# Kernel tuning notes

Hardware: AMD Instinct MI355X
Metric: run time of the kernel (lower is better)

The kernel has to match this reference:

```python
import jax, jax.numpy as jnp
import numpy as np

NUM_EXPERTS = 64
TOP_K = 2
AUX_LOSS_COEF = 0.01
Z_LOSS_COEF = 0.001


def setup_inputs() -> dict:
    key = jax.random.key(0)
    k1, k2 = jax.random.split(key)
    hidden_states = jax.random.normal(k1, (4, 4096, 4096), dtype=jnp.float32)
    # nn.Linear(hidden_size, num_experts, bias=False) -> weight [E, H]
    gate_w = jax.random.normal(k2, (NUM_EXPERTS, 4096), dtype=jnp.float32) * 0.02
    return {"hidden_states": hidden_states, "gate_w": gate_w}


def reference(hidden_states, gate_w):
    b, s, h = hidden_states.shape
    # gate projection: [b, s, E]
    router_logits = jnp.einsum("bsh,eh->bse", hidden_states, gate_w)
    # softmax in fp32 as in the torch module
    probs = jax.nn.softmax(router_logits.astype(jnp.float32), axis=-1)
    routing_weights, selected_experts = jax.lax.top_k(probs, TOP_K)
    routing_weights = routing_weights / jnp.sum(routing_weights, axis=-1, keepdims=True)
    routing_weights = routing_weights.astype(hidden_states.dtype)

    # auxiliary load-balancing loss
    num_tokens = b * s
    # scatter_(-1, selected, 1): top-k indices are distinct, so one_hot-sum == set-to-1
    expert_mask = jax.nn.one_hot(selected_experts, NUM_EXPERTS, dtype=router_logits.dtype).sum(axis=-2)  # [b,s,E]
    tokens_per_expert = expert_mask.sum(axis=(0, 1)) / num_tokens          # [E]
    router_prob_per_expert = probs.sum(axis=(0, 1)) / num_tokens           # [E]
    aux_loss = NUM_EXPERTS * jnp.sum(tokens_per_expert * router_prob_per_expert)

    # z-loss: mean of squared logsumexp over experts
    z_loss = jnp.mean(jax.scipy.special.logsumexp(router_logits, axis=-1) ** 2)

    router_loss = AUX_LOSS_COEF * aux_loss + Z_LOSS_COEF * z_loss
    return routing_weights, selected_experts, router_loss
```

## Files before the change

### kernel.cpp

```cpp
#include <hip/hip_runtime.h>
#include <math.h>

#define HDIM 4096
#define NEXP 64
#define NTOK 16384
#define MBLK 32
#define NCHUNK 64
#define CSTRIDE 68
#define GS_FLOATS 262144

typedef float v4f __attribute__((ext_vector_type(4)));
typedef short bh4 __attribute__((ext_vector_type(4)));
typedef float f32x16 __attribute__((ext_vector_type(16)));

#if defined(__has_builtin)
#if __has_builtin(__builtin_amdgcn_mfma_f32_32x32x8bf16_1k)
#define HAVE_MFMA_BUILTIN 1
#endif
#endif

__device__ __forceinline__ f32x16 mfma_bf16(bh4 a, bh4 b, f32x16 c) {
#ifdef HAVE_MFMA_BUILTIN
    return __builtin_amdgcn_mfma_f32_32x32x8bf16_1k(a, b, c, 0, 0, 0);
#else
    asm("v_mfma_f32_32x32x8_bf16 %0, %1, %2, %0" : "+v"(c) : "v"(a), "v"(b));
    return c;
#endif
}

__device__ __forceinline__ void barrier_lgkm_only() {
    asm volatile("s_waitcnt lgkmcnt(0)\n\ts_barrier" ::: "memory");
}

__device__ __forceinline__ void split2(float v, unsigned short& h0,
                                       unsigned short& h1) {
    unsigned b0 = __builtin_bit_cast(unsigned, v);
    unsigned r0 = (b0 + 0x7FFFu + ((b0 >> 16) & 1u)) & 0xFFFF0000u;
    h0 = (unsigned short)(r0 >> 16);
    float v1 = v - __builtin_bit_cast(float, r0);
    unsigned b1 = __builtin_bit_cast(unsigned, v1);
    h1 = (unsigned short)((b1 + 0x7FFFu + ((b1 >> 16) & 1u)) >> 16);
}

__device__ __forceinline__ uint2 pack4(const unsigned short* h) {
    return make_uint2((unsigned)h[0] | ((unsigned)h[1] << 16),
                      (unsigned)h[2] | ((unsigned)h[3] << 16));
}

__global__ __launch_bounds__(256) void gate_presplit(
    const float* __restrict__ gate, uint2* __restrict__ gs)
{
    const int f = blockIdx.x * 256 + threadIdx.x;
    const int l = f & 63;
    const int ntp = (f >> 6) & 1;
    const int k8g = f >> 7;
    const int e = ntp * 32 + (l & 31);
    const int k = k8g * 8 + (l >> 5) * 4;
    v4f x = *(const v4f*)&gate[(size_t)e * HDIM + k];
    float xv[4] = {x.x, x.y, x.z, x.w};
    unsigned short lo[4], hi[4];
#pragma unroll
    for (int j = 0; j < 4; ++j) split2(xv[j], lo[j], hi[j]);
    gs[((size_t)(k8g * 2 + 0) * 2 + ntp) * 64 + l] = pack4(lo);
    gs[((size_t)(k8g * 2 + 1) * 2 + ntp) * 64 + l] = pack4(hi);
}

__global__ __launch_bounds__(256, 4) void router_main(
    const float* __restrict__ hidden,
    const uint2* __restrict__ gs,
    float* __restrict__ out_rw,
    float* __restrict__ out_sel,
    float* __restrict__ psum_g,
    float* __restrict__ cnt_g,
    float* __restrict__ zsum_g)
{
    __shared__ uint2 Af[2][8][2][64];
    __shared__ float Pacc[2][16][64];
    __shared__ float C_lds[MBLK * CSTRIDE];
    __shared__ float rden[MBLK];
    __shared__ unsigned hist[NEXP];

    const int t = threadIdx.x;
    const int lane = t & 63;
    const int wave = __builtin_amdgcn_readfirstlane(t >> 6);
    const int ntp = wave & 1, h = wave >> 1;
    const int m0 = blockIdx.x * MBLK;

    const v4f* __restrict__ A4 = (const v4f*)hidden;

    const int row = t >> 3;
    const int k8s = t & 7;
    const size_t abase = (size_t)(m0 + row) * (HDIM / 4) + k8s * 2;
    const int sw_w = (k8s & 1) << 3;

    auto stageA = [&](int buf, v4f x0, v4f x1) {
        float av[8] = {x0.x, x0.y, x0.z, x0.w, x1.x, x1.y, x1.z, x1.w};
        unsigned short lo[8], hi[8];
#pragma unroll
        for (int u = 0; u < 8; ++u) split2(av[u], lo[u], hi[u]);
        const int s0 = row ^ sw_w;
        Af[buf][k8s][0][s0]      = pack4(lo);
        Af[buf][k8s][0][s0 + 32] = pack4(lo + 4);
        Af[buf][k8s][1][s0]      = pack4(hi);
        Af[buf][k8s][1][s0 + 32] = pack4(hi + 4);
    };

    f32x16 acc{};

    v4f ap0 = __builtin_nontemporal_load(&A4[abase]);
    v4f ap1 = __builtin_nontemporal_load(&A4[abase + 1]);
    stageA(0, ap0, ap1);
    ap0 = __builtin_nontemporal_load(&A4[abase + 16]);
    ap1 = __builtin_nontemporal_load(&A4[abase + 17]);

    uint2 bA[8], bB[8];
#pragma unroll
    for (int s = 0; s < 4; ++s) {
        const int k8g = h * 4 + s;
        bA[2 * s + 0] = gs[((size_t)(k8g * 2 + 0) * 2 + ntp) * 64 + lane];
        bA[2 * s + 1] = gs[((size_t)(k8g * 2 + 1) * 2 + ntp) * 64 + lane];
    }
    __syncthreads();

    auto step = [&](int it, uint2 (&bc)[8], uint2 (&bn)[8]) {
        const int cur = it & 1;
        const int cn = (it + 1 < NCHUNK) ? it + 1 : NCHUNK - 1;
#pragma unroll
        for (int s = 0; s < 4; ++s) {
            const int k8g = cn * 8 + h * 4 + s;
            bn[2 * s + 0] = gs[((size_t)(k8g * 2 + 0) * 2 + ntp) * 64 + lane];
            bn[2 * s + 1] = gs[((size_t)(k8g * 2 + 1) * 2 + ntp) * 64 + lane];
        }
        if (it + 1 < NCHUNK) stageA(cur ^ 1, ap0, ap1);
        const int ca = (it + 2 < NCHUNK) ? it + 2 : NCHUNK - 1;
        ap0 = __builtin_nontemporal_load(&A4[abase + (size_t)ca * 16]);
        ap1 = __builtin_nontemporal_load(&A4[abase + (size_t)ca * 16 + 1]);
#pragma unroll
        for (int s = 0; s < 4; ++s) {
            const int k8 = h * 4 + s;
            const int slot = lane ^ ((k8 & 1) << 3);
            bh4 a0 = __builtin_bit_cast(bh4, Af[cur][k8][0][slot]);
            bh4 a1 = __builtin_bit_cast(bh4, Af[cur][k8][1][slot]);
            bh4 b0 = __builtin_bit_cast(bh4, bc[2 * s + 0]);
            bh4 b1 = __builtin_bit_cast(bh4, bc[2 * s + 1]);
            acc = mfma_bf16(a0, b0, acc);
            acc = mfma_bf16(a1, b0, acc);
            acc = mfma_bf16(a0, b1, acc);
            acc = mfma_bf16(a1, b1, acc);
        }
        barrier_lgkm_only();
    };

    for (int it = 0; it < NCHUNK; it += 2) {
        step(it, bA, bB);
        step(it + 1, bB, bA);
    }

    asm volatile("s_nop 7\n\ts_nop 7" :::);

    if (h == 1) {
#pragma unroll
        for (int r = 0; r < 16; ++r) Pacc[ntp][r][lane] = acc[r];
    }
    if (t < NEXP) hist[t] = 0u;
    __syncthreads();
    if (h == 0) {
#pragma unroll
        for (int r = 0; r < 16; ++r) {
            float x = acc[r] + Pacc[ntp][r][lane];
            const int tok = (r & 3) + 8 * (r >> 2) + 4 * (lane >> 5);
            const int e = ntp * 32 + (lane & 31);
            C_lds[tok * CSTRIDE + e] = x;
        }
    }
    __syncthreads();

    if (wave != 0) return;

    float z = 0.f;
    if (lane < MBLK) {
        float v1 = -INFINITY, v2 = -INFINITY;
        int i1 = 0, i2 = 0;
        for (int e = 0; e < NEXP; ++e) {
            float v = C_lds[lane * CSTRIDE + e];
            if (v > v1)      { v2 = v1; i2 = i1; v1 = v; i1 = e; }
            else if (v > v2) { v2 = v;  i2 = e; }
        }
        atomicAdd(&hist[i1], 1u);
        atomicAdd(&hist[i2], 1u);

        float d = 0.f;
        for (int e = 0; e < NEXP; ++e) {
            float ev = expf(C_lds[lane * CSTRIDE + e] - v1);
            C_lds[lane * CSTRIDE + e] = ev;
            d += ev;
        }
        rden[lane] = 1.0f / d;
        float lse = v1 + logf(d);
        z = lse * lse;

        float e2 = expf(v2 - v1);
        float w2 = e2 / (1.f + e2);
        float w1 = 1.f - w2;
        int tok = m0 + lane;
        out_rw[2 * tok + 0] = w1;
        out_rw[2 * tok + 1] = w2;
        out_sel[2 * tok + 0] = (float)i1;
        out_sel[2 * tok + 1] = (float)i2;
    }

#pragma unroll
    for (int off = 32; off > 0; off >>= 1) z += __shfl_down(z, off);
    if (lane == 0) atomicAdd(zsum_g, z);

    float ps = 0.f;
    for (int m = 0; m < MBLK; ++m)
        ps += C_lds[m * CSTRIDE + lane] * rden[m];
    atomicAdd(&psum_g[lane], ps);
    atomicAdd(&cnt_g[lane], (float)hist[lane]);
}

__global__ void router_final(const float* __restrict__ ws, float* __restrict__ out_loss)
{
    int e = threadIdx.x;
    const float inv = 1.0f / (float)NTOK;
    float p = (ws[64 + e] * inv) * (ws[e] * inv);
#pragma unroll
    for (int off = 32; off > 0; off >>= 1) p += __shfl_down(p, off);
    if (e == 0)
        out_loss[0] = 0.01f * (64.f * p) + 0.001f * (ws[128] * inv);
}

extern "C" void kernel_launch(void* const* d_in, const int* in_sizes, int n_in,
                              void* d_out, int out_size, void* d_ws, size_t ws_size,
                              hipStream_t stream) {
    const float* hidden = (const float*)d_in[0];
    const float* gate   = (const float*)d_in[1];
    float* out = (float*)d_out;
    float* ws  = (float*)d_ws;
    float* stats = ws + GS_FLOATS;

    hipMemsetAsync(stats, 0, 129 * sizeof(float), stream);
    gate_presplit<<<dim3(256), dim3(256), 0, stream>>>(gate, (uint2*)ws);
    router_main<<<dim3(NTOK / MBLK), dim3(256), 0, stream>>>(
        hidden, (const uint2*)ws,
        out,
        out + NTOK * 2,
        stats, stats + 64, stats + 128);
    router_final<<<dim3(1), dim3(64), 0, stream>>>(stats, out + NTOK * 4);
}
```

Before: 402.2 us.

## Load A fragments directly into registers and split K across eight waves

Removes the LDS staging of the hidden-state tile and the per-chunk barrier. Each wave now loads its MFMA A fragment straight from global memory with a 4-deep register prefetch of both A and B. The block grows to 512 threads so that four waves split the K dimension, and their partial accumulators are reduced through LDS at the end. This trades coalesced row loads and shared-memory reuse for barrier-free streaming and more memory-level parallelism, at the cost of smaller, strided global accesses and higher register pressure.

```diff
diff --git a/kernel.cpp b/kernel.cpp
--- a/kernel.cpp
+++ b/kernel.cpp
@@ -5,7 +5,8 @@
 #define NEXP 64
 #define NTOK 16384
 #define MBLK 32
-#define NCHUNK 64
+#define STEPS 128
+#define PD 4
 #define CSTRIDE 68
 #define GS_FLOATS 262144
 
@@ -26,10 +27,6 @@
     asm("v_mfma_f32_32x32x8_bf16 %0, %1, %2, %0" : "+v"(c) : "v"(a), "v"(b));
     return c;
 #endif
-}
-
-__device__ __forceinline__ void barrier_lgkm_only() {
-    asm volatile("s_waitcnt lgkmcnt(0)\n\ts_barrier" ::: "memory");
 }
 
 __device__ __forceinline__ void split2(float v, unsigned short& h0,
@@ -65,7 +62,7 @@
     gs[((size_t)(k8g * 2 + 1) * 2 + ntp) * 64 + l] = pack4(hi);
 }
 
-__global__ __launch_bounds__(256, 4) void router_main(
+__global__ __launch_bounds__(512, 2) void router_main(
     const float* __restrict__ hidden,
     const uint2* __restrict__ gs,
     float* __restrict__ out_rw,
@@ -74,8 +71,7 @@
     float* __restrict__ cnt_g,
     float* __restrict__ zsum_g)
 {
-    __shared__ uint2 Af[2][8][2][64];
-    __shared__ float Pacc[2][16][64];
+    __shared__ float Pacc[3][2][16][64];
     __shared__ float C_lds[MBLK * CSTRIDE];
     __shared__ float rden[MBLK];
     __shared__ unsigned hist[NEXP];
@@ -86,91 +82,64 @@
     const int ntp = wave & 1, h = wave >> 1;
     const int m0 = blockIdx.x * MBLK;
 
-    const v4f* __restrict__ A4 = (const v4f*)hidden;
-
-    const int row = t >> 3;
-    const int k8s = t & 7;
-    const size_t abase = (size_t)(m0 + row) * (HDIM / 4) + k8s * 2;
-    const int sw_w = (k8s & 1) << 3;
-
-    auto stageA = [&](int buf, v4f x0, v4f x1) {
-        float av[8] = {x0.x, x0.y, x0.z, x0.w, x1.x, x1.y, x1.z, x1.w};
-        unsigned short lo[8], hi[8];
-#pragma unroll
-        for (int u = 0; u < 8; ++u) split2(av[u], lo[u], hi[u]);
-        const int s0 = row ^ sw_w;
-        Af[buf][k8s][0][s0]      = pack4(lo);
-        Af[buf][k8s][0][s0 + 32] = pack4(lo + 4);
-        Af[buf][k8s][1][s0]      = pack4(hi);
-        Af[buf][k8s][1][s0 + 32] = pack4(hi + 4);
-    };
+    const int tok = lane & 31;
+    const int kj = (lane >> 5) * 4;
+
+    const float* Abase = hidden + (size_t)(m0 + tok) * HDIM + h * (HDIM / 4) + kj;
+    const uint2* Bbase = gs + (size_t)h * 128 * 256 + ntp * 64 + lane;
 
     f32x16 acc{};
 
-    v4f ap0 = __builtin_nontemporal_load(&A4[abase]);
-    v4f ap1 = __builtin_nontemporal_load(&A4[abase + 1]);
-    stageA(0, ap0, ap1);
-    ap0 = __builtin_nontemporal_load(&A4[abase + 16]);
-    ap1 = __builtin_nontemporal_load(&A4[abase + 17]);
-
-    uint2 bA[8], bB[8];
-#pragma unroll
-    for (int s = 0; s < 4; ++s) {
-        const int k8g = h * 4 + s;
-        bA[2 * s + 0] = gs[((size_t)(k8g * 2 + 0) * 2 + ntp) * 64 + lane];
-        bA[2 * s + 1] = gs[((size_t)(k8g * 2 + 1) * 2 + ntp) * 64 + lane];
-    }
-    __syncthreads();
-
-    auto step = [&](int it, uint2 (&bc)[8], uint2 (&bn)[8]) {
-        const int cur = it & 1;
-        const int cn = (it + 1 < NCHUNK) ? it + 1 : NCHUNK - 1;
-#pragma unroll
-        for (int s = 0; s < 4; ++s) {
-            const int k8g = cn * 8 + h * 4 + s;
-            bn[2 * s + 0] = gs[((size_t)(k8g * 2 + 0) * 2 + ntp) * 64 + lane];
-            bn[2 * s + 1] = gs[((size_t)(k8g * 2 + 1) * 2 + ntp) * 64 + lane];
-        }
-        if (it + 1 < NCHUNK) stageA(cur ^ 1, ap0, ap1);
-        const int ca = (it + 2 < NCHUNK) ? it + 2 : NCHUNK - 1;
-        ap0 = __builtin_nontemporal_load(&A4[abase + (size_t)ca * 16]);
-        ap1 = __builtin_nontemporal_load(&A4[abase + (size_t)ca * 16 + 1]);
-#pragma unroll
-        for (int s = 0; s < 4; ++s) {
-            const int k8 = h * 4 + s;
-            const int slot = lane ^ ((k8 & 1) << 3);
-            bh4 a0 = __builtin_bit_cast(bh4, Af[cur][k8][0][slot]);
-            bh4 a1 = __builtin_bit_cast(bh4, Af[cur][k8][1][slot]);
-            bh4 b0 = __builtin_bit_cast(bh4, bc[2 * s + 0]);
-            bh4 b1 = __builtin_bit_cast(bh4, bc[2 * s + 1]);
-            acc = mfma_bf16(a0, b0, acc);
-            acc = mfma_bf16(a1, b0, acc);
-            acc = mfma_bf16(a0, b1, acc);
-            acc = mfma_bf16(a1, b1, acc);
-        }
-        barrier_lgkm_only();
-    };
-
-    for (int it = 0; it < NCHUNK; it += 2) {
-        step(it, bA, bB);
-        step(it + 1, bB, bA);
+    v4f apf[PD];
+    uint2 b0f[PD], b1f[PD];
+#pragma unroll
+    for (int i = 0; i < PD; ++i) {
+        apf[i] = *(const v4f*)(Abase + (size_t)i * 8);
+        b0f[i] = Bbase[(size_t)i * 256];
+        b1f[i] = Bbase[(size_t)i * 256 + 128];
+    }
+
+    for (int s = 0; s < STEPS; s += PD) {
+#pragma unroll
+        for (int u = 0; u < PD; ++u) {
+            v4f a = apf[u];
+            uint2 b0 = b0f[u], b1 = b1f[u];
+            int sn = s + u + PD;
+            sn = (sn < STEPS) ? sn : (STEPS - 1);
+            apf[u] = *(const v4f*)(Abase + (size_t)sn * 8);
+            b0f[u] = Bbase[(size_t)sn * 256];
+            b1f[u] = Bbase[(size_t)sn * 256 + 128];
+            float av[4] = {a.x, a.y, a.z, a.w};
+            unsigned short lo[4], hi[4];
+#pragma unroll
+            for (int j = 0; j < 4; ++j) split2(av[j], lo[j], hi[j]);
+            bh4 a0 = __builtin_bit_cast(bh4, pack4(lo));
+            bh4 a1 = __builtin_bit_cast(bh4, pack4(hi));
+            bh4 bb0 = __builtin_bit_cast(bh4, b0);
+            bh4 bb1 = __builtin_bit_cast(bh4, b1);
+            acc = mfma_bf16(a0, bb0, acc);
+            acc = mfma_bf16(a1, bb0, acc);
+            acc = mfma_bf16(a0, bb1, acc);
+            acc = mfma_bf16(a1, bb1, acc);
+        }
     }
 
     asm volatile("s_nop 7\n\ts_nop 7" :::);
 
-    if (h == 1) {
-#pragma unroll
-        for (int r = 0; r < 16; ++r) Pacc[ntp][r][lane] = acc[r];
+    if (h > 0) {
+#pragma unroll
+        for (int r = 0; r < 16; ++r) Pacc[h - 1][ntp][r][lane] = acc[r];
     }
     if (t < NEXP) hist[t] = 0u;
     __syncthreads();
     if (h == 0) {
 #pragma unroll
         for (int r = 0; r < 16; ++r) {
-            float x = acc[r] + Pacc[ntp][r][lane];
-            const int tok = (r & 3) + 8 * (r >> 2) + 4 * (lane >> 5);
+            float x = acc[r] + Pacc[0][ntp][r][lane] + Pacc[1][ntp][r][lane]
+                             + Pacc[2][ntp][r][lane];
+            const int to = (r & 3) + 8 * (r >> 2) + 4 * (lane >> 5);
             const int e = ntp * 32 + (lane & 31);
-            C_lds[tok * CSTRIDE + e] = x;
+            C_lds[to * CSTRIDE + e] = x;
         }
     }
     __syncthreads();
@@ -202,11 +171,11 @@
         float e2 = expf(v2 - v1);
         float w2 = e2 / (1.f + e2);
         float w1 = 1.f - w2;
-        int tok = m0 + lane;
-        out_rw[2 * tok + 0] = w1;
-        out_rw[2 * tok + 1] = w2;
-        out_sel[2 * tok + 0] = (float)i1;
-        out_sel[2 * tok + 1] = (float)i2;
+        int tk = m0 + lane;
+        out_rw[2 * tk + 0] = w1;
+        out_rw[2 * tk + 1] = w2;
+        out_sel[2 * tk + 0] = (float)i1;
+        out_sel[2 * tk + 1] = (float)i2;
     }
 
 #pragma unroll
@@ -242,7 +211,7 @@
 
     hipMemsetAsync(stats, 0, 129 * sizeof(float), stream);
     gate_presplit<<<dim3(256), dim3(256), 0, stream>>>(gate, (uint2*)ws);
-    router_main<<<dim3(NTOK / MBLK), dim3(256), 0, stream>>>(
+    router_main<<<dim3(NTOK / MBLK), dim3(512), 0, stream>>>(
         hidden, (const uint2*)ws,
         out,
         out + NTOK * 2,
```

Measured after the change: 422.1 us. 5.0% more time.
